# Kernel tuning notes

Hardware: AMD Instinct MI355X
Metric: run time of the kernel (lower is better)

Reference implementation:

```python
import jax, jax.numpy as jnp
import numpy as np

N_USERS = 100000
N_ENTITY = 100000
D = 64
N_RK = 3
B = 16384
LA = 20   # authors per user
LC = 5    # genres per user


def setup_inputs() -> dict:
    key = jax.random.key(0)
    ks = jax.random.split(key, 6)
    return {
        "user_id": jax.random.randint(ks[0], (B,), 0, N_USERS),
        "artists_id": jax.random.randint(ks[1], (B, LA), 0, N_ENTITY),
        "categories_id": jax.random.randint(ks[2], (B, LC), 0, N_ENTITY),
        "rate": 0,  # dropout prob; eval mode -> identity
        "user_factors": jax.random.normal(ks[3], (N_USERS, D), jnp.float32),
        "entity_factors": jax.random.normal(ks[4], (N_ENTITY, D), jnp.float32),
        "relation_k": jax.random.normal(ks[5], (D, N_RK), jnp.float32),
    }


def _contrib(idx, users, entity_factors):
    # idx: [B, L] entity indices; users: [B, D]
    emb = entity_factors[idx]                      # [B, L, D] gather
    pre = jnp.einsum("bld,bd->bl", emb, users)     # per-aspect mat-vec (niubi)
    return pre.mean(axis=1), pre                   # mean over segment -> [B]


def reference(user_id, artists_id, categories_id, rate, user_factors,
              entity_factors, relation_k):
    users = user_factors[user_id]                               # [B, D]
    # importance of each aspect type
    scores = jax.nn.softmax(
        jax.nn.leaky_relu(users @ relation_k, negative_slope=0.2), axis=1)  # [B, 3]
    s_act = scores[:, 0]
    s_dir = scores[:, 1]
    # contribution of each aspect (ragged gather-matvec-mean, vectorized)
    c_act, niubi_act = _contrib(artists_id, users, entity_factors)
    c_dir, niubi_dir = _contrib(categories_id, users, entity_factors)
    importance_sum = s_act + s_dir
    prediction = (c_act * s_act + c_dir * s_dir) / importance_sum
    return prediction, scores, c_act, c_dir, niubi_act, niubi_dir
```

## Files before the change

kernel.cpp:

```cpp
#include <hip/hip_runtime.h>

constexpr int B  = 16384;
constexpr int D  = 64;
constexpr int LA = 20;
constexpr int LC = 5;

template <int CTRL>
__device__ __forceinline__ float ror_add(float v) {
    const int r = __builtin_amdgcn_update_dpp(
        0, __float_as_int(v), CTRL, 0xF, 0xF, true);
    return v + __int_as_float(r);
}

template <int N>
__device__ __forceinline__ void reduce16(float (&p)[N]) {
    #pragma unroll
    for (int l = 0; l < N; ++l) p[l] = ror_add<0x128>(p[l]);
    #pragma unroll
    for (int l = 0; l < N; ++l) p[l] = ror_add<0x124>(p[l]);
    #pragma unroll
    for (int l = 0; l < N; ++l) p[l] = ror_add<0x122>(p[l]);
    #pragma unroll
    for (int l = 0; l < N; ++l) p[l] = ror_add<0x121>(p[l]);
}

__global__ __launch_bounds__(256, 4) void aspect_kernel(
    const int*   __restrict__ user_id,
    const int*   __restrict__ artists_id,
    const int*   __restrict__ categories_id,
    const float* __restrict__ user_factors,
    const float* __restrict__ entity_factors,
    const float* __restrict__ relation_k,
    float*       __restrict__ out)
{
    const int tid = threadIdx.x;
    const int sl  = tid & 15;
    const int grp = tid >> 4;
    const int b   = (blockIdx.x << 4) + grp;

    float* pred    = out;
    float* scores  = out + B;
    float* c_act_o = out + (size_t)4 * B;
    float* c_dir_o = out + (size_t)5 * B;
    float* niubiA  = out + (size_t)6 * B;
    float* niubiC  = niubiA + (size_t)B * LA;

    const int    uid = user_id[b];
    const float4 u4  = *(const float4*)&user_factors[(size_t)uid * D + sl * 4];

    float ps[3];
    {
        const int d0 = sl * 4;
        ps[0] = fmaf(u4.x, relation_k[(d0+0)*3+0], fmaf(u4.y, relation_k[(d0+1)*3+0],
                fmaf(u4.z, relation_k[(d0+2)*3+0], u4.w * relation_k[(d0+3)*3+0])));
        ps[1] = fmaf(u4.x, relation_k[(d0+0)*3+1], fmaf(u4.y, relation_k[(d0+1)*3+1],
                fmaf(u4.z, relation_k[(d0+2)*3+1], u4.w * relation_k[(d0+3)*3+1])));
        ps[2] = fmaf(u4.x, relation_k[(d0+0)*3+2], fmaf(u4.y, relation_k[(d0+1)*3+2],
                fmaf(u4.z, relation_k[(d0+2)*3+2], u4.w * relation_k[(d0+3)*3+2])));
    }
    reduce16(ps);
    float q0 = ps[0] >= 0.f ? ps[0] : 0.2f * ps[0];
    float q1 = ps[1] >= 0.f ? ps[1] : 0.2f * ps[1];
    float q2 = ps[2] >= 0.f ? ps[2] : 0.2f * ps[2];
    const float m   = fmaxf(q0, fmaxf(q1, q2));
    const float e0  = __expf(q0 - m), e1 = __expf(q1 - m), e2 = __expf(q2 - m);
    const float inv = 1.f / (e0 + e1 + e2);
    const float s0 = e0 * inv, s1 = e1 * inv, s2 = e2 * inv;

    float pa[LA];
    #pragma unroll
    for (int l = 0; l < LA; ++l) {
        const int    idx = artists_id[b * LA + l];
        const float4 e   = *(const float4*)&entity_factors[(size_t)idx * D + sl * 4];
        pa[l] = fmaf(e.x, u4.x, fmaf(e.y, u4.y, fmaf(e.z, u4.z, e.w * u4.w)));
    }
    reduce16(pa);
    float sumA = 0.f;
    #pragma unroll
    for (int l = 0; l < LA; ++l) sumA += pa[l];
    const float c_act = sumA * (1.f / LA);

    float pc[LC];
    #pragma unroll
    for (int l = 0; l < LC; ++l) {
        const int    idx = categories_id[b * LC + l];
        const float4 e   = *(const float4*)&entity_factors[(size_t)idx * D + sl * 4];
        pc[l] = fmaf(e.x, u4.x, fmaf(e.y, u4.y, fmaf(e.z, u4.z, e.w * u4.w)));
    }
    reduce16(pc);
    float sumC = 0.f;
    #pragma unroll
    for (int l = 0; l < LC; ++l) sumC += pc[l];
    const float c_dir = sumC * (1.f / LC);

    if (sl < 5) {
        float4 v;
        v.x = sl == 0 ? pa[0] : sl == 1 ? pa[4]  : sl == 2 ? pa[8]  : sl == 3 ? pa[12] : pa[16];
        v.y = sl == 0 ? pa[1] : sl == 1 ? pa[5]  : sl == 2 ? pa[9]  : sl == 3 ? pa[13] : pa[17];
        v.z = sl == 0 ? pa[2] : sl == 1 ? pa[6]  : sl == 2 ? pa[10] : sl == 3 ? pa[14] : pa[18];
        v.w = sl == 0 ? pa[3] : sl == 1 ? pa[7]  : sl == 2 ? pa[11] : sl == 3 ? pa[15] : pa[19];
        *(float4*)&niubiA[(size_t)b * LA + sl * 4] = v;
    }
    if (sl < LC) {
        const float v = sl == 0 ? pc[0] : sl == 1 ? pc[1] : sl == 2 ? pc[2] : sl == 3 ? pc[3] : pc[4];
        niubiC[(size_t)b * LC + sl] = v;
    }
    if (sl < 3) {
        const float v = sl == 0 ? s0 : sl == 1 ? s1 : s2;
        scores[b * 3 + sl] = v;
    }
    if (sl == 0) {
        pred[b]    = (c_act * s0 + c_dir * s1) / (s0 + s1);
        c_act_o[b] = c_act;
        c_dir_o[b] = c_dir;
    }
}

extern "C" void kernel_launch(void* const* d_in, const int* in_sizes, int n_in,
                              void* d_out, int out_size, void* d_ws, size_t ws_size,
                              hipStream_t stream) {
    const int*   user_id        = (const int*)d_in[0];
    const int*   artists_id     = (const int*)d_in[1];
    const int*   categories_id  = (const int*)d_in[2];
    const float* user_factors   = (const float*)d_in[4];
    const float* entity_factors = (const float*)d_in[5];
    const float* relation_k     = (const float*)d_in[6];
    float*       out            = (float*)d_out;

    const int rows_per_block = 16;
    const int grid = B / rows_per_block;
    aspect_kernel<<<grid, 256, 0, stream>>>(
        user_id, artists_id, categories_id, user_factors, entity_factors, relation_k, out);
}
```

Baseline: 104.0 us.

## Use 32 lanes per row with float2 gathers and swizzle reduction

Changes the thread mapping from 16 lanes per batch row to 32 lanes, so each lane gathers float2 instead of float4 entity slices, and adds a ds_swizzle step to reduce across 32 lanes. Artist indices are loaded as int4 vectors, and the niubi stores are moved right after each reduction. Occupancy hint is raised to 8 blocks per CU and the grid doubles. This aims to raise memory-level parallelism for the random gathers, at the cost of an extra cross-lane reduction step and smaller per-lane loads.

```diff
diff --git a/kernel.cpp b/kernel.cpp
--- a/kernel.cpp
+++ b/kernel.cpp
@@ -5,15 +5,20 @@
 constexpr int LA = 20;
 constexpr int LC = 5;
 
+template <int PAT>
+__device__ __forceinline__ float swz(float v) {
+    return __int_as_float(__builtin_amdgcn_ds_swizzle(__float_as_int(v), PAT));
+}
 template <int CTRL>
 __device__ __forceinline__ float ror_add(float v) {
-    const int r = __builtin_amdgcn_update_dpp(
-        0, __float_as_int(v), CTRL, 0xF, 0xF, true);
+    const int r = __builtin_amdgcn_update_dpp(0, __float_as_int(v), CTRL, 0xF, 0xF, true);
     return v + __int_as_float(r);
 }
 
 template <int N>
-__device__ __forceinline__ void reduce16(float (&p)[N]) {
+__device__ __forceinline__ void reduce32(float (&p)[N]) {
+    #pragma unroll
+    for (int l = 0; l < N; ++l) p[l] += swz<0x401F>(p[l]);
     #pragma unroll
     for (int l = 0; l < N; ++l) p[l] = ror_add<0x128>(p[l]);
     #pragma unroll
@@ -24,7 +29,7 @@
     for (int l = 0; l < N; ++l) p[l] = ror_add<0x121>(p[l]);
 }
 
-__global__ __launch_bounds__(256, 4) void aspect_kernel(
+__global__ __launch_bounds__(256, 8) void aspect_kernel(
     const int*   __restrict__ user_id,
     const int*   __restrict__ artists_id,
     const int*   __restrict__ categories_id,
@@ -34,9 +39,9 @@
     float*       __restrict__ out)
 {
     const int tid = threadIdx.x;
-    const int sl  = tid & 15;
-    const int grp = tid >> 4;
-    const int b   = (blockIdx.x << 4) + grp;
+    const int sl  = tid & 31;
+    const int grp = tid >> 5;
+    const int b   = (blockIdx.x << 3) + grp;
 
     float* pred    = out;
     float* scores  = out + B;
@@ -46,19 +51,59 @@
     float* niubiC  = niubiA + (size_t)B * LA;
 
     const int    uid = user_id[b];
-    const float4 u4  = *(const float4*)&user_factors[(size_t)uid * D + sl * 4];
+    const float2 u2  = *(const float2*)&user_factors[(size_t)uid * D + sl * 2];
+
+    const int4* aidv = (const int4*)&artists_id[(size_t)b * LA];
+    float pa[LA];
+    #pragma unroll
+    for (int k = 0; k < 5; ++k) {
+        const int4 aw = aidv[k];
+        const int idx[4] = {aw.x, aw.y, aw.z, aw.w};
+        #pragma unroll
+        for (int j = 0; j < 4; ++j) {
+            const float2 e = *(const float2*)&entity_factors[(size_t)idx[j] * D + sl * 2];
+            pa[k * 4 + j] = fmaf(e.x, u2.x, e.y * u2.y);
+        }
+    }
+    reduce32(pa);
+    float sumA = 0.f;
+    #pragma unroll
+    for (int l = 0; l < LA; ++l) sumA += pa[l];
+    if (sl < 5) {
+        float4 v;
+        v.x = sl == 0 ? pa[0] : sl == 1 ? pa[4]  : sl == 2 ? pa[8]  : sl == 3 ? pa[12] : pa[16];
+        v.y = sl == 0 ? pa[1] : sl == 1 ? pa[5]  : sl == 2 ? pa[9]  : sl == 3 ? pa[13] : pa[17];
+        v.z = sl == 0 ? pa[2] : sl == 1 ? pa[6]  : sl == 2 ? pa[10] : sl == 3 ? pa[14] : pa[18];
+        v.w = sl == 0 ? pa[3] : sl == 1 ? pa[7]  : sl == 2 ? pa[11] : sl == 3 ? pa[15] : pa[19];
+        *(float4*)&niubiA[(size_t)b * LA + sl * 4] = v;
+    }
+    const float c_act = sumA * (1.f / LA);
+
+    float pc[LC];
+    #pragma unroll
+    for (int l = 0; l < LC; ++l) {
+        const int    idx = categories_id[b * LC + l];
+        const float2 e   = *(const float2*)&entity_factors[(size_t)idx * D + sl * 2];
+        pc[l] = fmaf(e.x, u2.x, e.y * u2.y);
+    }
+    reduce32(pc);
+    float sumC = 0.f;
+    #pragma unroll
+    for (int l = 0; l < LC; ++l) sumC += pc[l];
+    if (sl < LC) {
+        const float v = sl == 0 ? pc[0] : sl == 1 ? pc[1] : sl == 2 ? pc[2] : sl == 3 ? pc[3] : pc[4];
+        niubiC[(size_t)b * LC + sl] = v;
+    }
+    const float c_dir = sumC * (1.f / LC);
 
     float ps[3];
     {
-        const int d0 = sl * 4;
-        ps[0] = fmaf(u4.x, relation_k[(d0+0)*3+0], fmaf(u4.y, relation_k[(d0+1)*3+0],
-                fmaf(u4.z, relation_k[(d0+2)*3+0], u4.w * relation_k[(d0+3)*3+0])));
-        ps[1] = fmaf(u4.x, relation_k[(d0+0)*3+1], fmaf(u4.y, relation_k[(d0+1)*3+1],
-                fmaf(u4.z, relation_k[(d0+2)*3+1], u4.w * relation_k[(d0+3)*3+1])));
-        ps[2] = fmaf(u4.x, relation_k[(d0+0)*3+2], fmaf(u4.y, relation_k[(d0+1)*3+2],
-                fmaf(u4.z, relation_k[(d0+2)*3+2], u4.w * relation_k[(d0+3)*3+2])));
+        const int d0 = sl * 2;
+        ps[0] = fmaf(u2.x, relation_k[(d0+0)*3+0], u2.y * relation_k[(d0+1)*3+0]);
+        ps[1] = fmaf(u2.x, relation_k[(d0+0)*3+1], u2.y * relation_k[(d0+1)*3+1]);
+        ps[2] = fmaf(u2.x, relation_k[(d0+0)*3+2], u2.y * relation_k[(d0+1)*3+2]);
     }
-    reduce16(ps);
+    reduce32(ps);
     float q0 = ps[0] >= 0.f ? ps[0] : 0.2f * ps[0];
     float q1 = ps[1] >= 0.f ? ps[1] : 0.2f * ps[1];
     float q2 = ps[2] >= 0.f ? ps[2] : 0.2f * ps[2];
@@ -67,44 +112,6 @@
     const float inv = 1.f / (e0 + e1 + e2);
     const float s0 = e0 * inv, s1 = e1 * inv, s2 = e2 * inv;
 
-    float pa[LA];
-    #pragma unroll
-    for (int l = 0; l < LA; ++l) {
-        const int    idx = artists_id[b * LA + l];
-        const float4 e   = *(const float4*)&entity_factors[(size_t)idx * D + sl * 4];
-        pa[l] = fmaf(e.x, u4.x, fmaf(e.y, u4.y, fmaf(e.z, u4.z, e.w * u4.w)));
-    }
-    reduce16(pa);
-    float sumA = 0.f;
-    #pragma unroll
-    for (int l = 0; l < LA; ++l) sumA += pa[l];
-    const float c_act = sumA * (1.f / LA);
-
-    float pc[LC];
-    #pragma unroll
-    for (int l = 0; l < LC; ++l) {
-        const int    idx = categories_id[b * LC + l];
-        const float4 e   = *(const float4*)&entity_factors[(size_t)idx * D + sl * 4];
-        pc[l] = fmaf(e.x, u4.x, fmaf(e.y, u4.y, fmaf(e.z, u4.z, e.w * u4.w)));
-    }
-    reduce16(pc);
-    float sumC = 0.f;
-    #pragma unroll
-    for (int l = 0; l < LC; ++l) sumC += pc[l];
-    const float c_dir = sumC * (1.f / LC);
-
-    if (sl < 5) {
-        float4 v;
-        v.x = sl == 0 ? pa[0] : sl == 1 ? pa[4]  : sl == 2 ? pa[8]  : sl == 3 ? pa[12] : pa[16];
-        v.y = sl == 0 ? pa[1] : sl == 1 ? pa[5]  : sl == 2 ? pa[9]  : sl == 3 ? pa[13] : pa[17];
-        v.z = sl == 0 ? pa[2] : sl == 1 ? pa[6]  : sl == 2 ? pa[10] : sl == 3 ? pa[14] : pa[18];
-        v.w = sl == 0 ? pa[3] : sl == 1 ? pa[7]  : sl == 2 ? pa[11] : sl == 3 ? pa[15] : pa[19];
-        *(float4*)&niubiA[(size_t)b * LA + sl * 4] = v;
-    }
-    if (sl < LC) {
-        const float v = sl == 0 ? pc[0] : sl == 1 ? pc[1] : sl == 2 ? pc[2] : sl == 3 ? pc[3] : pc[4];
-        niubiC[(size_t)b * LC + sl] = v;
-    }
     if (sl < 3) {
         const float v = sl == 0 ? s0 : sl == 1 ? s1 : s2;
         scores[b * 3 + sl] = v;
@@ -127,7 +134,7 @@
     const float* relation_k     = (const float*)d_in[6];
     float*       out            = (float*)d_out;
 
-    const int rows_per_block = 16;
+    const int rows_per_block = 8;
     const int grid = B / rows_per_block;
     aspect_kernel<<<grid, 256, 0, stream>>>(
         user_id, artists_id, categories_id, user_factors, entity_factors, relation_k, out);
```

After: 104.9 us. About the same (+0.9%).
